# Kernel tuning notes

Measured on AMD Instinct MI355X. Metric: run time of the kernel, lower is better.

The kernel has to match this reference:

```python
import jax, jax.numpy as jnp
import numpy as np

N_HEADS = 4


def grid_sample_bilinear(img, grid):
    # img: (B, C, H, W); grid: (B, *S, 2) with (x, y) in [-1, 1]; torch bilinear, align_corners=True
    B, C, H, W = img.shape
    sp = grid.shape[1:-1]
    g = grid.reshape(B, -1, 2)
    x = (g[..., 0] + 1.0) * 0.5 * (W - 1)
    y = (g[..., 1] + 1.0) * 0.5 * (H - 1)
    x0 = jnp.floor(x)
    y0 = jnp.floor(y)
    wx = x - x0
    wy = y - y0
    x0i = jnp.clip(x0, 0, W - 1).astype(jnp.int32)
    x1i = jnp.clip(x0 + 1, 0, W - 1).astype(jnp.int32)
    y0i = jnp.clip(y0, 0, H - 1).astype(jnp.int32)
    y1i = jnp.clip(y0 + 1, 0, H - 1).astype(jnp.int32)
    flat = img.reshape(B, C, H * W)
    take = jax.vmap(lambda f, i: f[:, i])  # (C, HW), (N,) -> (C, N)
    out = (take(flat, y0i * W + x0i) * ((1 - wx) * (1 - wy))[:, None, :]
           + take(flat, y0i * W + x1i) * (wx * (1 - wy))[:, None, :]
           + take(flat, y1i * W + x0i) * ((1 - wx) * wy)[:, None, :]
           + take(flat, y1i * W + x1i) * (wx * wy)[:, None, :])
    return out.reshape((B, C) + sp)


def dw_conv_k4s4(x, w, b):
    # depthwise conv, kernel=4, stride=4, pad=0 (kernel == stride): non-overlapping patches
    B, C, H, W = x.shape
    xr = x.reshape(B, C, H // 4, 4, W // 4, 4)
    return jnp.einsum('bchpwq,cpq->bchw', xr, w) + b[None, :, None, None]


def ln_channels(x, g, b, eps=1e-5):
    # LayerNormProxy: LayerNorm over channel dim of NCHW
    mu = jnp.mean(x, axis=1, keepdims=True)
    var = jnp.var(x, axis=1, keepdims=True)
    return (x - mu) * jax.lax.rsqrt(var + eps) * g[None, :, None, None] + b[None, :, None, None]


def ref_points(Hk, Wk):
    ry = jnp.linspace(0.5, Hk - 0.5, Hk) / (Hk - 1.0) * 2.0 - 1.0
    rx = jnp.linspace(0.5, Wk - 0.5, Wk) / (Wk - 1.0) * 2.0 - 1.0
    return jnp.stack(jnp.meshgrid(ry, rx, indexing='ij'), axis=-1)  # (Hk, Wk, 2) as (y, x)


def q_grid(H, W):
    ry = jnp.arange(H, dtype=jnp.float32) / (H - 1.0) * 2.0 - 1.0
    rx = jnp.arange(W, dtype=jnp.float32) / (W - 1.0) * 2.0 - 1.0
    return jnp.stack(jnp.meshgrid(ry, rx, indexing='ij'), axis=-1).reshape(H * W, 2)


def dat_block(x, p):
    # DAttentionBaseline: n_groups=1, stride=ksize=4, offset_range_factor=-1, use_pe (learned rpe table)
    dw_w, dw_b, ln_g, ln_b, pw_w, wq, bq, wk, bk, wv, bv, wo, bo, rpe = p
    B, C, H, W = x.shape
    hc = C // N_HEADS
    scale = hc ** -0.5
    q = jnp.einsum('oc,bchw->bohw', wq, x) + bq[None, :, None, None]
    t = jax.nn.gelu(ln_channels(dw_conv_k4s4(q, dw_w, dw_b), ln_g, ln_b), approximate=False)
    off = jnp.einsum('oc,bchw->bohw', pw_w, t)  # (B, 2, Hk, Wk), channels = (dy, dx)
    Hk, Wk = off.shape[2], off.shape[3]
    ns = Hk * Wk
    pos = jnp.clip(off.transpose(0, 2, 3, 1) + ref_points(Hk, Wk)[None], -1.0, 1.0)  # (B,Hk,Wk,2) (y,x)
    xs = grid_sample_bilinear(x, pos[..., ::-1]).reshape(B, C, ns)  # kv == q input here
    k = jnp.einsum('oc,bcn->bon', wk, xs) + bk[None, :, None]
    v = jnp.einsum('oc,bcn->bon', wv, xs) + bv[None, :, None]
    qh = q.reshape(B, N_HEADS, hc, H * W)
    attn = jnp.einsum('bhcm,bhcn->bhmn', qh, k.reshape(B, N_HEADS, hc, ns)) * scale
    disp = (q_grid(H, W)[None, :, None, :] - pos.reshape(B, 1, ns, 2)) * 0.5  # (B, HW, ns, 2) (y,x)
    rpe_b = jnp.broadcast_to(rpe[None], (B,) + rpe.shape)
    attn = attn + grid_sample_bilinear(rpe_b, disp[..., ::-1])  # (B, heads, HW, ns)
    attn = jax.nn.softmax(attn, axis=-1)
    out = jnp.einsum('bhmn,bhcn->bhcm', attn, v.reshape(B, N_HEADS, hc, ns)).reshape(B, C, H, W)
    return jnp.einsum('oc,bchw->bohw', wo, out) + bo[None, :, None, None]


def _block_params(key, c, H, W):
    ks = jax.random.split(key, 7)
    return dict(
        off_dw_w=0.05 * jax.random.normal(ks[0], (c, 4, 4), dtype=jnp.float32),
        off_dw_b=jnp.zeros((c,), jnp.float32),
        ln_g=jnp.ones((c,), jnp.float32),
        ln_b=jnp.zeros((c,), jnp.float32),
        off_pw_w=0.02 * jax.random.normal(ks[1], (2, c), dtype=jnp.float32),
        wq=0.02 * jax.random.normal(ks[2], (c, c), dtype=jnp.float32),
        bq=jnp.zeros((c,), jnp.float32),
        wk=0.02 * jax.random.normal(ks[3], (c, c), dtype=jnp.float32),
        bk=jnp.zeros((c,), jnp.float32),
        wv=0.02 * jax.random.normal(ks[4], (c, c), dtype=jnp.float32),
        bv=jnp.zeros((c,), jnp.float32),
        wo=0.02 * jax.random.normal(ks[5], (c, c), dtype=jnp.float32),
        bo=jnp.zeros((c,), jnp.float32),
        rpe=0.01 * jax.random.normal(ks[6], (N_HEADS, 2 * H - 1, 2 * W - 1), dtype=jnp.float32),
    )


def setup_inputs() -> dict:
    key = jax.random.key(0)
    k0, k1, k2 = jax.random.split(key, 3)
    B, C, H, W = 8, 512, 64, 64
    inp = {'x0': jax.random.normal(k0, (B, C, H, W), dtype=jnp.float32)}
    for pre, k in (('sc_', k1), ('tr_', k2)):
        for n, v in _block_params(k, C // 2, H, W).items():
            inp[pre + n] = v
    return inp


def reference(x0,
              sc_off_dw_w, sc_off_dw_b, sc_ln_g, sc_ln_b, sc_off_pw_w, sc_wq, sc_bq, sc_wk, sc_bk,
              sc_wv, sc_bv, sc_wo, sc_bo, sc_rpe,
              tr_off_dw_w, tr_off_dw_b, tr_ln_g, tr_ln_b, tr_off_pw_w, tr_wq, tr_bq, tr_wk, tr_bk,
              tr_wv, tr_bv, tr_wo, tr_bo, tr_rpe):
    B, C, H, W = x0.shape
    qc1 = C // 2
    q = x0[:, :qc1]
    sc_p = (sc_off_dw_w, sc_off_dw_b, sc_ln_g, sc_ln_b, sc_off_pw_w, sc_wq, sc_bq, sc_wk, sc_bk,
            sc_wv, sc_bv, sc_wo, sc_bo, sc_rpe)
    tr_p = (tr_off_dw_w, tr_off_dw_b, tr_ln_g, tr_ln_b, tr_off_pw_w, tr_wq, tr_bq, tr_wk, tr_bk,
            tr_wv, tr_bv, tr_wo, tr_bo, tr_rpe)
    s = dat_block(q, sc_p)
    t = dat_block(q, tr_p)
    z = jnp.zeros((B, C - qc1, H, W), x0.dtype)
    scale_full = jnp.concatenate([z, s], axis=1)
    trans_full = jnp.concatenate([z, t], axis=1)
    res = x0 * jnp.exp(scale_full) + trans_full
    jac = jnp.sum(scale_full, axis=(1, 2, 3))[None, :]  # (n_vars=1, B)
    return res, jac
```

## Files before the change

### kernel.cpp

```cpp
#include <hip/hip_runtime.h>
#include <math.h>

typedef __bf16 bf16;
typedef __attribute__((ext_vector_type(8))) __bf16 bf16x8;
typedef __attribute__((ext_vector_type(4))) __bf16 bf16x4;
typedef __attribute__((ext_vector_type(4))) float floatx4;

#define MFMA16(a, b, c) __builtin_amdgcn_mfma_f32_16x16x32_bf16((a), (b), (c), 0, 0, 0)

__device__ __forceinline__ float bflo(unsigned d) {
    unsigned u = d << 16; float f; __builtin_memcpy(&f, &u, 4); return f;
}
__device__ __forceinline__ float bfhi(unsigned d) {
    unsigned u = d & 0xffff0000u; float f; __builtin_memcpy(&f, &u, 4); return f;
}

__device__ __forceinline__ void breduce1(float &a, float* lds, int t) {
    #pragma unroll
    for (int off = 32; off; off >>= 1) a += __shfl_xor(a, off, 64);
    __syncthreads();
    if ((t & 63) == 0) lds[t >> 6] = a;
    __syncthreads();
    a = lds[0] + lds[1] + lds[2] + lds[3];
}

__global__ __launch_bounds__(256) void init_kernel(const float* __restrict__ x0,
                                                   float* __restrict__ out) {
    int fi = blockIdx.x * 256 + threadIdx.x;
    int b = fi >> 18;
    int r = fi & 262143;
    const float4* src = (const float4*)x0;
    float4* dst = (float4*)out;
    dst[(size_t)b * 524288 + r] = src[(size_t)b * 524288 + r];
}

__global__ __launch_bounds__(256) void wconv(
    const float* __restrict__ w0, const float* __restrict__ w1,
    const float* __restrict__ w2, const float* __restrict__ w3,
    const float* __restrict__ w4, const float* __restrict__ w5,
    const float* __restrict__ w6, const float* __restrict__ w7,
    bf16* __restrict__ dst) {
    const int wi = blockIdx.y;
    const float* src = wi == 0 ? w0 : wi == 1 ? w1 : wi == 2 ? w2 : wi == 3 ? w3
                     : wi == 4 ? w4 : wi == 5 ? w5 : wi == 6 ? w6 : w7;
    const int i = blockIdx.x * 1024 + threadIdx.x * 4;
    const float4 v = *(const float4*)(src + i);
    bf16x4 h, l;
    #pragma unroll
    for (int j = 0; j < 4; j++) {
        const float f = ((const float*)&v)[j];
        const bf16 hb = (bf16)f;
        h[j] = hb;
        l[j] = (bf16)(f - (float)hb);
    }
    *(bf16x4*)(dst + (size_t)wi * 65536 + i) = h;
    *(bf16x4*)(dst + (size_t)(8 + wi) * 65536 + i) = l;
}

template <int MODE>
__global__ __launch_bounds__(256) void gemm_mfma(
    const void* __restrict__ Aptr, int ldA, long long bsA,
    const bf16* __restrict__ Whi, const bf16* __restrict__ Wlo,
    const float* __restrict__ bias,
    bf16* __restrict__ outb,
    float* outf,
    const float* __restrict__ x0full,
    float* __restrict__ jpart)
{
    constexpr bool ASPLIT = (MODE <= 2);
    __shared__ __align__(16) bf16 As_hi[128 * 40];
    __shared__ __align__(16) bf16 As_lo[ASPLIT ? 128 * 40 : 1];
    __shared__ __align__(16) bf16 Bs_hi[128 * 40];
    __shared__ __align__(16) bf16 Bs_lo[128 * 40];
    __shared__ float red[4];
    const int t = threadIdx.x;
    const int b = blockIdx.z;
    const int n0 = blockIdx.x * 128;
    const int o0 = blockIdx.y * 128;
    const int w = t >> 6, l = t & 63;
    const int wr = w & 1, wc = w >> 1;
    const int lr = l & 15, lq = l >> 4;

    floatx4 acc[4][4] = {};

    for (int kb = 0; kb < 8; kb++) {
        if (ASPLIT) {
            const float* Af = (const float*)Aptr + (size_t)b * bsA;
            #pragma unroll
            for (int s = 0; s < 4; s++) {
                const int kk = s * 8 + (t >> 5);
                const int n = (t & 31) * 4;
                const float4 v = *(const float4*)(Af + (size_t)(kb * 32 + kk) * ldA + n0 + n);
                #pragma unroll
                for (int j = 0; j < 4; j++) {
                    const float f = ((const float*)&v)[j];
                    const bf16 hb = (bf16)f;
                    As_hi[(n + j) * 40 + kk] = hb;
                    As_lo[(n + j) * 40 + kk] = (bf16)(f - (float)hb);
                }
            }
        } else {
            const bf16* Ab = (const bf16*)Aptr + (size_t)b * bsA;
            #pragma unroll
            for (int s = 0; s < 2; s++) {
                const int idx = t + 256 * s;
                const int row = idx >> 2, seg = idx & 3;
                *(bf16x8*)(As_hi + row * 40 + seg * 8) =
                    *(const bf16x8*)(Ab + (size_t)(n0 + row) * 256 + kb * 32 + seg * 8);
            }
        }
        #pragma unroll
        for (int s = 0; s < 2; s++) {
            const int idx = t + 256 * s;
            const int row = idx >> 2, seg = idx & 3;
            *(bf16x8*)(Bs_hi + row * 40 + seg * 8) =
                *(const bf16x8*)(Whi + (size_t)(o0 + row) * 256 + kb * 32 + seg * 8);
            *(bf16x8*)(Bs_lo + row * 40 + seg * 8) =
                *(const bf16x8*)(Wlo + (size_t)(o0 + row) * 256 + kb * 32 + seg * 8);
        }
        __syncthreads();
        bf16x8 ah[4], al[4], bh[4], bl[4];
        #pragma unroll
        for (int f = 0; f < 4; f++) {
            ah[f] = *(const bf16x8*)(As_hi + (wr * 64 + f * 16 + lr) * 40 + lq * 8);
            if (ASPLIT)
                al[f] = *(const bf16x8*)(As_lo + (wr * 64 + f * 16 + lr) * 40 + lq * 8);
            bh[f] = *(const bf16x8*)(Bs_hi + (wc * 64 + f * 16 + lr) * 40 + lq * 8);
            bl[f] = *(const bf16x8*)(Bs_lo + (wc * 64 + f * 16 + lr) * 40 + lq * 8);
        }
        #pragma unroll
        for (int i = 0; i < 4; i++)
            #pragma unroll
            for (int j = 0; j < 4; j++) {
                acc[i][j] = MFMA16(ah[i], bh[j], acc[i][j]);
                acc[i][j] = MFMA16(ah[i], bl[j], acc[i][j]);
                if (ASPLIT) acc[i][j] = MFMA16(al[i], bh[j], acc[i][j]);
            }
        __syncthreads();
    }

    float ssum = 0.0f;
    #pragma unroll
    for (int i = 0; i < 4; i++) {
        #pragma unroll
        for (int j = 0; j < 4; j++) {
            const int o_g = o0 + wc * 64 + j * 16 + lr;
            const int n_b = n0 + wr * 64 + i * 16 + lq * 4;
            const float bia = bias[o_g];
            floatx4 val = acc[i][j];
            val[0] += bia; val[1] += bia; val[2] += bia; val[3] += bia;
            if (MODE == 0) {
                *(floatx4*)(outf + (size_t)b * 2097152 + (size_t)o_g * 4096 + n_b) = val;
                #pragma unroll
                for (int r = 0; r < 4; r++)
                    outb[((size_t)b * 4096 + n_b + r) * 256 + o_g] = (bf16)val[r];
            } else if (MODE == 1) {
                #pragma unroll
                for (int r = 0; r < 4; r++)
                    outb[((size_t)b * 256 + n_b + r) * 256 + o_g] = (bf16)val[r];
            } else if (MODE == 2) {
                bf16x4 pv;
                pv[0] = (bf16)val[0]; pv[1] = (bf16)val[1];
                pv[2] = (bf16)val[2]; pv[3] = (bf16)val[3];
                *(bf16x4*)(outb + ((size_t)b * 256 + o_g) * 256 + n_b) = pv;
            } else {
                const size_t addr = (size_t)b * 2097152 + (size_t)(256 + o_g) * 4096 + n_b;
                if (MODE == 3) {
                    *(floatx4*)(outf + addr) = val;
                } else {
                    const floatx4 s4 = *(const floatx4*)(outf + addr);
                    const floatx4 x4 = *(const floatx4*)(x0full + addr);
                    floatx4 res;
                    #pragma unroll
                    for (int r = 0; r < 4; r++) res[r] = x4[r] * expf(s4[r]) + val[r];
                    *(floatx4*)(outf + addr) = res;
                    ssum += s4[0] + s4[1] + s4[2] + s4[3];
                }
            }
        }
    }
    if (MODE == 4) {
        breduce1(ssum, red, t);
        if (t == 0) jpart[b * 64 + blockIdx.y * 32 + blockIdx.x] = ssum;
    }
}

__global__ __launch_bounds__(64) void jac_reduce(const float* __restrict__ jpart,
                                                 float* __restrict__ out) {
    const int b = blockIdx.x, t = threadIdx.x;
    float v = jpart[b * 64 + t];
    #pragma unroll
    for (int off = 32; off; off >>= 1) v += __shfl_xor(v, off, 64);
    if (t == 0) out[16777216 + b] = v;
}

__global__ __launch_bounds__(256) void offset_kernel(
    const float* __restrict__ q,
    const float* __restrict__ dw_w, const float* __restrict__ dw_b,
    const float* __restrict__ ln_g, const float* __restrict__ ln_b,
    const float* __restrict__ pw_w,
    float* __restrict__ pos)
{
    __shared__ float red[8];
    const int wk = blockIdx.x, hk = blockIdx.y, b = blockIdx.z;
    const int c = threadIdx.x;
    const float* qp = q + (size_t)b * 2097152 + (size_t)c * 4096 + (hk * 4) * 64 + wk * 4;
    float accv = dw_b[c];
    #pragma unroll
    for (int p = 0; p < 4; p++) {
        const float4 r = *(const float4*)(qp + p * 64);
        const float4 w = *(const float4*)(dw_w + c * 16 + p * 4);
        accv += r.x * w.x + r.y * w.y + r.z * w.z + r.w * w.w;
    }
    float a = accv, sq = accv * accv;
    #pragma unroll
    for (int off = 32; off; off >>= 1) {
        a += __shfl_xor(a, off, 64);
        sq += __shfl_xor(sq, off, 64);
    }
    __syncthreads();
    if ((c & 63) == 0) { red[c >> 6] = a; red[4 + (c >> 6)] = sq; }
    __syncthreads();
    a = red[0] + red[1] + red[2] + red[3];
    sq = red[4] + red[5] + red[6] + red[7];
    const float mu = a * (1.0f / 256.0f);
    const float var = sq * (1.0f / 256.0f) - mu * mu;
    float nrm = (accv - mu) * rsqrtf(var + 1e-5f) * ln_g[c] + ln_b[c];
    const float act = 0.5f * nrm * (1.0f + erff(nrm * 0.70710678118654752f));
    float v0 = pw_w[c] * act;
    float v1 = pw_w[256 + c] * act;
    #pragma unroll
    for (int off = 32; off; off >>= 1) {
        v0 += __shfl_xor(v0, off, 64);
        v1 += __shfl_xor(v1, off, 64);
    }
    __syncthreads();
    if ((c & 63) == 0) { red[c >> 6] = v0; red[4 + (c >> 6)] = v1; }
    __syncthreads();
    if (c == 0) {
        v0 = red[0] + red[1] + red[2] + red[3];
        v1 = red[4] + red[5] + red[6] + red[7];
        const float refy = (0.5f + hk) * (2.0f / 15.0f) - 1.0f;
        const float refx = (0.5f + wk) * (2.0f / 15.0f) - 1.0f;
        const float py = fminf(fmaxf(v0 + refy, -1.0f), 1.0f);
        const float px = fminf(fmaxf(v1 + refx, -1.0f), 1.0f);
        const int n = hk * 16 + wk;
        pos[(b * 256 + n) * 2] = py;
        pos[(b * 256 + n) * 2 + 1] = px;
    }
}

__global__ __launch_bounds__(256) void sample_kernel(
    const float* __restrict__ x0,
    const float* __restrict__ pos,
    float* __restrict__ xs)
{
    const int c = threadIdx.x, n = blockIdx.x, b = blockIdx.y;
    const float py = pos[(b * 256 + n) * 2];
    const float px = pos[(b * 256 + n) * 2 + 1];
    const float x = (px + 1.0f) * 31.5f;
    const float y = (py + 1.0f) * 31.5f;
    const float xf = floorf(x), yf = floorf(y);
    const float wx = x - xf, wy = y - yf;
    const int xi0 = min(max((int)xf, 0), 63);
    const int xi1 = min(xi0 + 1, 63);
    const int yi0 = min(max((int)yf, 0), 63);
    const int yi1 = min(yi0 + 1, 63);
    const float* base = x0 + (size_t)b * 2097152 + (size_t)c * 4096;
    const float v00 = base[yi0 * 64 + xi0], v01 = base[yi0 * 64 + xi1];
    const float v10 = base[yi1 * 64 + xi0], v11 = base[yi1 * 64 + xi1];
    xs[((size_t)b * 256 + c) * 256 + n] =
        v00 * (1 - wx) * (1 - wy) + v01 * wx * (1 - wy) +
        v10 * (1 - wx) * wy + v11 * wx * wy;
}

__global__ __launch_bounds__(256, 4) void attn_mfma(
    const bf16* qbfT,
    const bf16* __restrict__ kT,
    const bf16* __restrict__ vb,
    const float* __restrict__ pos,
    const float* __restrict__ rpe,
    bf16* obfT)
{
    __shared__ __align__(16) bf16 pl[16896];
    __shared__ float wxs[256];
    const int t = threadIdx.x;
    const int w = t >> 6, l = t & 63;
    const int lr = l & 15, lq = l >> 4;
    const int m_base = blockIdx.x * 64 + w * 16;
    const int my = blockIdx.x;
    const int h = blockIdx.y, b = blockIdx.z;

    const float2 pp = *(const float2*)(pos + (b * 256 + t) * 2);
    const float yy = (float)my + 63.0f - 31.5f * pp.x;
    const float xo = 63.0f - 31.5f * pp.y;
    const float yfl = floorf(yy);
    const float wy_r = yy - yfl;
    const int y0 = min((int)yfl, 126);
    const int o0_r = y0 * 127;
    const int o1_r = min(y0 + 1, 126) * 127;
    const int xb_r = (int)floorf(xo);
    wxs[t] = xo - (float)xb_r;

    const float* rp = rpe + h * 16129;

    const bf16* qrow = qbfT + ((size_t)b * 4096 + m_base + lr) * 256 + h * 64;
    const bf16x8 qf0 = *(const bf16x8*)(qrow + lq * 8);
    const bf16x8 qf1 = *(const bf16x8*)(qrow + 32 + lq * 8);

    #pragma unroll 4
    for (int i = 0; i < 64; i++) {
        const int xb = __shfl(xb_r, i);
        const float wy = __shfl(wy_r, i);
        const int o0 = __shfl(o0_r, i);
        const int o1 = __shfl(o1_r, i);
        const int xj = min(xb + l, 126);
        const float v0 = rp[o0 + xj];
        const float v1 = rp[o1 + xj];
        pl[(w * 64 + i) * 66 + l] = (bf16)fmaf(wy, v1 - v0, v0);
    }
    {
        const int xe = min(xb_r + 64, 126);
        const float e0 = rp[o0_r + xe];
        const float e1 = rp[o1_r + xe];
        pl[t * 66 + 64] = (bf16)fmaf(wy_r, e1 - e0, e0);
    }

    floatx4 lg[16];
    #pragma unroll
    for (int nf = 0; nf < 16; nf++) {
        const bf16* krow = kT + ((size_t)b * 256 + nf * 16 + lr) * 256 + h * 64;
        const bf16x8 k0 = *(const bf16x8*)(krow + lq * 8);
        const bf16x8 k1 = *(const bf16x8*)(krow + 32 + lq * 8);
        floatx4 a = {};
        a = MFMA16(qf0, k0, a);
        a = MFMA16(qf1, k1, a);
        lg[nf] = a;
    }

    __syncthreads();

    #pragma unroll
    for (int nf = 0; nf < 16; nf++) {
        const int n = nf * 16 + lr;
        const unsigned* rw = (const unsigned*)(pl + n * 66 + w * 16 + lq * 4);
        const unsigned d0 = rw[0], d1 = rw[1], d2 = rw[2];
        float rv[5];
        rv[0] = bflo(d0); rv[1] = bfhi(d0);
        rv[2] = bflo(d1); rv[3] = bfhi(d1);
        rv[4] = bflo(d2);
        const float wxv = wxs[n];
        #pragma unroll
        for (int r = 0; r < 4; r++)
            lg[nf][r] = lg[nf][r] * 0.125f + (rv[r] + wxv * (rv[r + 1] - rv[r]));
    }

    float mx[4], inv[4];
    #pragma unroll
    for (int r = 0; r < 4; r++) {
        float m = -1e30f;
        #pragma unroll
        for (int nf = 0; nf < 16; nf++) m = fmaxf(m, lg[nf][r]);
        #pragma unroll
        for (int off = 1; off < 16; off <<= 1) m = fmaxf(m, __shfl_xor(m, off, 64));
        mx[r] = m;
    }
    #pragma unroll
    for (int r = 0; r < 4; r++) {
        float s = 0.0f;
        #pragma unroll
        for (int nf = 0; nf < 16; nf++) {
            const float e = __expf(lg[nf][r] - mx[r]);
            lg[nf][r] = e;
            s += e;
        }
        #pragma unroll
        for (int off = 1; off < 16; off <<= 1) s += __shfl_xor(s, off, 64);
        inv[r] = 1.0f / s;
    }

    __syncthreads();

    bf16* plw = pl + w * 16 * 264;
    #pragma unroll
    for (int nf = 0; nf < 16; nf++)
        #pragma unroll
        for (int r = 0; r < 4; r++)
            plw[(lq * 4 + r) * 264 + nf * 16 + lr] = (bf16)(lg[nf][r] * inv[r]);

    floatx4 oc[4] = {};
    #pragma unroll
    for (int kf = 0; kf < 8; kf++) {
        const bf16x8 pa = *(const bf16x8*)(plw + lr * 264 + kf * 32 + lq * 8);
        #pragma unroll
        for (int j = 0; j < 4; j++) {
            const bf16x8 vf = *(const bf16x8*)(
                vb + ((size_t)b * 256 + h * 64 + j * 16 + lr) * 256 + kf * 32 + lq * 8);
            oc[j] = MFMA16(pa, vf, oc[j]);
        }
    }

    #pragma unroll
    for (int j = 0; j < 4; j++)
        #pragma unroll
        for (int r = 0; r < 4; r++)
            obfT[((size_t)b * 4096 + m_base + lq * 4 + r) * 256 + h * 64 + j * 16 + lr]
                = (bf16)oc[j][r];
}

extern "C" void kernel_launch(void* const* d_in, const int* in_sizes, int n_in,
                              void* d_out, int out_size, void* d_ws, size_t ws_size,
                              hipStream_t stream) {
    const float* x0 = (const float*)d_in[0];
    float* out = (float*)d_out;
    float* ws = (float*)d_ws;
    bf16* qbfT  = (bf16*)ws;
    float* xsT  = ws + 4194304;
    bf16* kTb   = (bf16*)(ws + 4718592);
    bf16* vbb   = (bf16*)(ws + 4980736);
    bf16* wbf   = (bf16*)(ws + 5242880);
    float* pos  = ws + 5767168;
    float* jpart= ws + 5771264;

    wconv<<<dim3(64, 8), 256, 0, stream>>>(
        (const float*)d_in[6], (const float*)d_in[8], (const float*)d_in[10],
        (const float*)d_in[12], (const float*)d_in[20], (const float*)d_in[22],
        (const float*)d_in[24], (const float*)d_in[26], wbf);

    for (int pass = 0; pass < 2; pass++) {
        const int pb = 1 + 14 * pass;
        const float* dw_w = (const float*)d_in[pb + 0];
        const float* dw_b = (const float*)d_in[pb + 1];
        const float* ln_g = (const float*)d_in[pb + 2];
        const float* ln_b = (const float*)d_in[pb + 3];
        const float* pw_w = (const float*)d_in[pb + 4];
        const float* bq   = (const float*)d_in[pb + 6];
        const float* bk   = (const float*)d_in[pb + 8];
        const float* bv   = (const float*)d_in[pb + 10];
        const float* bo   = (const float*)d_in[pb + 12];
        const float* rpe  = (const float*)d_in[pb + 13];
        const bf16* wq_h = wbf + (size_t)(pass * 4 + 0) * 65536;
        const bf16* wk_h = wbf + (size_t)(pass * 4 + 1) * 65536;
        const bf16* wv_h = wbf + (size_t)(pass * 4 + 2) * 65536;
        const bf16* wo_h = wbf + (size_t)(pass * 4 + 3) * 65536;
        const bf16* wq_l = wq_h + 8 * 65536;
        const bf16* wk_l = wk_h + 8 * 65536;
        const bf16* wv_l = wv_h + 8 * 65536;
        const bf16* wo_l = wo_h + 8 * 65536;

        gemm_mfma<0><<<dim3(32, 2, 8), 256, 0, stream>>>(
            x0, 4096, 2097152LL, wq_h, wq_l, bq, qbfT, out, nullptr, nullptr);
        offset_kernel<<<dim3(16, 16, 8), 256, 0, stream>>>(
            out, dw_w, dw_b, ln_g, ln_b, pw_w, pos);
        sample_kernel<<<dim3(256, 8), 256, 0, stream>>>(x0, pos, xsT);
        gemm_mfma<1><<<dim3(2, 2, 8), 256, 0, stream>>>(
            xsT, 256, 65536LL, wk_h, wk_l, bk, kTb, nullptr, nullptr, nullptr);
        gemm_mfma<2><<<dim3(2, 2, 8), 256, 0, stream>>>(
            xsT, 256, 65536LL, wv_h, wv_l, bv, vbb, nullptr, nullptr, nullptr);
        attn_mfma<<<dim3(64, 4, 8), 256, 0, stream>>>(
            qbfT, kTb, vbb, pos, rpe, qbfT);
        if (pass == 0)
            gemm_mfma<3><<<dim3(32, 2, 8), 256, 0, stream>>>(
                qbfT, 256, 1048576LL, wo_h, wo_l, bo, nullptr, out, nullptr, nullptr);
        else
            gemm_mfma<4><<<dim3(32, 2, 8), 256, 0, stream>>>(
                qbfT, 256, 1048576LL, wo_h, wo_l, bo, nullptr, out, x0, jpart);
    }
    init_kernel<<<8192, 256, 0, stream>>>(x0, out);
    jac_reduce<<<8, 64, 0, stream>>>(jpart, out);
}
```

Before: 687.5 us.

## Fuse K/V projection GEMMs, pre-split sampled features to bf16, coalesce attention output

The sample kernel now writes the bilinearly sampled features as a hi/lo bf16 pair in transposed (token-major) layout, so the separate K and V projection launches can merge into one gemm_kv kernel that consumes split-bf16 operands directly. Attention output is staged through LDS and written as 16-byte vectors instead of scattered 2-byte stores. The first V fragments are prefetched before the barrier, and the rpe interpolation loop is unrolled further. This removes one launch and the fp32 conversion inside the GEMM, at the cost of more LDS traffic and registers in the attention kernel.

After: 615.1 us. 1.12x faster.

```diff
diff --git a/kernel.cpp b/kernel.cpp
--- a/kernel.cpp
+++ b/kernel.cpp
@@ -154,15 +154,6 @@
                 #pragma unroll
                 for (int r = 0; r < 4; r++)
                     outb[((size_t)b * 4096 + n_b + r) * 256 + o_g] = (bf16)val[r];
-            } else if (MODE == 1) {
-                #pragma unroll
-                for (int r = 0; r < 4; r++)
-                    outb[((size_t)b * 256 + n_b + r) * 256 + o_g] = (bf16)val[r];
-            } else if (MODE == 2) {
-                bf16x4 pv;
-                pv[0] = (bf16)val[0]; pv[1] = (bf16)val[1];
-                pv[2] = (bf16)val[2]; pv[3] = (bf16)val[3];
-                *(bf16x4*)(outb + ((size_t)b * 256 + o_g) * 256 + n_b) = pv;
             } else {
                 const size_t addr = (size_t)b * 2097152 + (size_t)(256 + o_g) * 4096 + n_b;
                 if (MODE == 3) {
@@ -185,6 +176,87 @@
     }
 }
 
+__global__ __launch_bounds__(256) void gemm_kv(
+    const bf16* __restrict__ xs_hi, const bf16* __restrict__ xs_lo,
+    const bf16* __restrict__ wkh, const bf16* __restrict__ wkl,
+    const bf16* __restrict__ wvh, const bf16* __restrict__ wvl,
+    const float* __restrict__ bk, const float* __restrict__ bv,
+    bf16* __restrict__ kT, bf16* __restrict__ vbuf)
+{
+    __shared__ __align__(16) bf16 As_hi[128 * 40];
+    __shared__ __align__(16) bf16 As_lo[128 * 40];
+    __shared__ __align__(16) bf16 Bs_hi[128 * 40];
+    __shared__ __align__(16) bf16 Bs_lo[128 * 40];
+    const int t = threadIdx.x;
+    const int b = blockIdx.z;
+    const int n0 = blockIdx.x * 128;
+    const int kv = blockIdx.y >> 1;
+    const int o0 = (blockIdx.y & 1) * 128;
+    const bf16* Whi = kv ? wvh : wkh;
+    const bf16* Wlo = kv ? wvl : wkl;
+    const float* bias = kv ? bv : bk;
+    const int w = t >> 6, l = t & 63;
+    const int wr = w & 1, wc = w >> 1;
+    const int lr = l & 15, lq = l >> 4;
+
+    floatx4 acc[4][4] = {};
+
+    for (int kb = 0; kb < 8; kb++) {
+        #pragma unroll
+        for (int s = 0; s < 2; s++) {
+            const int idx = t + 256 * s;
+            const int row = idx >> 2, seg = idx & 3;
+            const size_t asrc = ((size_t)b * 256 + n0 + row) * 256 + kb * 32 + seg * 8;
+            *(bf16x8*)(As_hi + row * 40 + seg * 8) = *(const bf16x8*)(xs_hi + asrc);
+            *(bf16x8*)(As_lo + row * 40 + seg * 8) = *(const bf16x8*)(xs_lo + asrc);
+            *(bf16x8*)(Bs_hi + row * 40 + seg * 8) =
+                *(const bf16x8*)(Whi + (size_t)(o0 + row) * 256 + kb * 32 + seg * 8);
+            *(bf16x8*)(Bs_lo + row * 40 + seg * 8) =
+                *(const bf16x8*)(Wlo + (size_t)(o0 + row) * 256 + kb * 32 + seg * 8);
+        }
+        __syncthreads();
+        bf16x8 ah[4], al[4], bh[4], bl[4];
+        #pragma unroll
+        for (int f = 0; f < 4; f++) {
+            ah[f] = *(const bf16x8*)(As_hi + (wr * 64 + f * 16 + lr) * 40 + lq * 8);
+            al[f] = *(const bf16x8*)(As_lo + (wr * 64 + f * 16 + lr) * 40 + lq * 8);
+            bh[f] = *(const bf16x8*)(Bs_hi + (wc * 64 + f * 16 + lr) * 40 + lq * 8);
+            bl[f] = *(const bf16x8*)(Bs_lo + (wc * 64 + f * 16 + lr) * 40 + lq * 8);
+        }
+        #pragma unroll
+        for (int i = 0; i < 4; i++)
+            #pragma unroll
+            for (int j = 0; j < 4; j++) {
+                acc[i][j] = MFMA16(ah[i], bh[j], acc[i][j]);
+                acc[i][j] = MFMA16(ah[i], bl[j], acc[i][j]);
+                acc[i][j] = MFMA16(al[i], bh[j], acc[i][j]);
+            }
+        __syncthreads();
+    }
+
+    #pragma unroll
+    for (int i = 0; i < 4; i++) {
+        #pragma unroll
+        for (int j = 0; j < 4; j++) {
+            const int o_g = o0 + wc * 64 + j * 16 + lr;
+            const int n_b = n0 + wr * 64 + i * 16 + lq * 4;
+            const float bia = bias[o_g];
+            floatx4 val = acc[i][j];
+            val[0] += bia; val[1] += bia; val[2] += bia; val[3] += bia;
+            if (kv == 0) {
+                #pragma unroll
+                for (int r = 0; r < 4; r++)
+                    kT[((size_t)b * 256 + n_b + r) * 256 + o_g] = (bf16)val[r];
+            } else {
+                bf16x4 pv;
+                pv[0] = (bf16)val[0]; pv[1] = (bf16)val[1];
+                pv[2] = (bf16)val[2]; pv[3] = (bf16)val[3];
+                *(bf16x4*)(vbuf + ((size_t)b * 256 + o_g) * 256 + n_b) = pv;
+            }
+        }
+    }
+}
+
 __global__ __launch_bounds__(64) void jac_reduce(const float* __restrict__ jpart,
                                                  float* __restrict__ out) {
     const int b = blockIdx.x, t = threadIdx.x;
@@ -253,7 +325,8 @@
 __global__ __launch_bounds__(256) void sample_kernel(
     const float* __restrict__ x0,
     const float* __restrict__ pos,
-    float* __restrict__ xs)
+    bf16* __restrict__ xs_hi,
+    bf16* __restrict__ xs_lo)
 {
     const int c = threadIdx.x, n = blockIdx.x, b = blockIdx.y;
     const float py = pos[(b * 256 + n) * 2];
@@ -269,9 +342,13 @@
     const float* base = x0 + (size_t)b * 2097152 + (size_t)c * 4096;
     const float v00 = base[yi0 * 64 + xi0], v01 = base[yi0 * 64 + xi1];
     const float v10 = base[yi1 * 64 + xi0], v11 = base[yi1 * 64 + xi1];
-    xs[((size_t)b * 256 + c) * 256 + n] =
+    const float f =
         v00 * (1 - wx) * (1 - wy) + v01 * wx * (1 - wy) +
         v10 * (1 - wx) * wy + v11 * wx * wy;
+    const bf16 hb = (bf16)f;
+    const size_t addr = ((size_t)b * 256 + n) * 256 + c;
+    xs_hi[addr] = hb;
+    xs_lo[addr] = (bf16)(f - (float)hb);
 }
 
 __global__ __launch_bounds__(256, 4) void attn_mfma(
@@ -308,7 +385,7 @@
     const bf16x8 qf0 = *(const bf16x8*)(qrow + lq * 8);
     const bf16x8 qf1 = *(const bf16x8*)(qrow + 32 + lq * 8);
 
-    #pragma unroll 4
+    #pragma unroll 8
     for (int i = 0; i < 64; i++) {
         const int xb = __shfl(xb_r, i);
         const float wy = __shfl(wy_r, i);
@@ -338,6 +415,14 @@
         lg[nf] = a;
     }
 
+    bf16x8 vpre[2][4];
+    #pragma unroll
+    for (int kf = 0; kf < 2; kf++)
+        #pragma unroll
+        for (int j = 0; j < 4; j++)
+            vpre[kf][j] = *(const bf16x8*)(
+                vb + ((size_t)b * 256 + h * 64 + j * 16 + lr) * 256 + kf * 32 + lq * 8);
+
     __syncthreads();
 
     #pragma unroll
@@ -394,18 +479,24 @@
         const bf16x8 pa = *(const bf16x8*)(plw + lr * 264 + kf * 32 + lq * 8);
         #pragma unroll
         for (int j = 0; j < 4; j++) {
-            const bf16x8 vf = *(const bf16x8*)(
+            const bf16x8 vf = (kf < 2) ? vpre[kf][j] : *(const bf16x8*)(
                 vb + ((size_t)b * 256 + h * 64 + j * 16 + lr) * 256 + kf * 32 + lq * 8);
             oc[j] = MFMA16(pa, vf, oc[j]);
         }
     }
 
+    bf16* ot = plw;
     #pragma unroll
     for (int j = 0; j < 4; j++)
         #pragma unroll
         for (int r = 0; r < 4; r++)
-            obfT[((size_t)b * 4096 + m_base + lq * 4 + r) * 256 + h * 64 + j * 16 + lr]
-                = (bf16)oc[j][r];
+            ot[(lq * 4 + r) * 72 + j * 16 + lr] = (bf16)oc[j][r];
+    const int mrow = l >> 2, seg = l & 3;
+    const bf16x8 ov0 = *(const bf16x8*)(ot + mrow * 72 + seg * 8);
+    const bf16x8 ov1 = *(const bf16x8*)(ot + mrow * 72 + (4 + seg) * 8);
+    bf16* orow = obfT + ((size_t)b * 4096 + m_base + mrow) * 256 + h * 64;
+    *(bf16x8*)(orow + seg * 8) = ov0;
+    *(bf16x8*)(orow + (4 + seg) * 8) = ov1;
 }
 
 extern "C" void kernel_launch(void* const* d_in, const int* in_sizes, int n_in,
@@ -415,7 +506,8 @@
     float* out = (float*)d_out;
     float* ws = (float*)d_ws;
     bf16* qbfT  = (bf16*)ws;
-    float* xsT  = ws + 4194304;
+    bf16* xs_hi = (bf16*)(ws + 4194304);
+    bf16* xs_lo = xs_hi + 524288;
     bf16* kTb   = (bf16*)(ws + 4718592);
     bf16* vbb   = (bf16*)(ws + 4980736);
     bf16* wbf   = (bf16*)(ws + 5242880);
@@ -452,11 +544,9 @@
             x0, 4096, 2097152LL, wq_h, wq_l, bq, qbfT, out, nullptr, nullptr);
         offset_kernel<<<dim3(16, 16, 8), 256, 0, stream>>>(
             out, dw_w, dw_b, ln_g, ln_b, pw_w, pos);
-        sample_kernel<<<dim3(256, 8), 256, 0, stream>>>(x0, pos, xsT);
-        gemm_mfma<1><<<dim3(2, 2, 8), 256, 0, stream>>>(
-            xsT, 256, 65536LL, wk_h, wk_l, bk, kTb, nullptr, nullptr, nullptr);
-        gemm_mfma<2><<<dim3(2, 2, 8), 256, 0, stream>>>(
-            xsT, 256, 65536LL, wv_h, wv_l, bv, vbb, nullptr, nullptr, nullptr);
+        sample_kernel<<<dim3(256, 8), 256, 0, stream>>>(x0, pos, xs_hi, xs_lo);
+        gemm_kv<<<dim3(2, 4, 8), 256, 0, stream>>>(
+            xs_hi, xs_lo, wk_h, wk_l, wv_h, wv_l, bk, bv, kTb, vbb);
         attn_mfma<<<dim3(64, 4, 8), 256, 0, stream>>>(
             qbfT, kTb, vbb, pos, rpe, qbfT);
         if (pass == 0)
```
